# Kernel optimization log

Measured on AMD Instinct MI355X. Metric: run time of the kernel, lower is better.

The kernel has to match this reference:

```python
import jax, jax.numpy as jnp
import numpy as np

N_HEAD = 16
ROPE_BASE = 10000.0


def _rope_cache(T, head_dim):
    # half-split RoPE: cos/sin of shape [T, head_dim//2]
    half = head_dim // 2
    inv_freq = ROPE_BASE ** (-jnp.arange(half, dtype=jnp.float32) / half)
    angles = jnp.arange(T, dtype=jnp.float32)[:, None] * inv_freq[None, :]  # [T, half]
    return jnp.cos(angles), jnp.sin(angles)


def _apply_rope(x, cos, sin):
    # x: [B, H, T, D]; cos/sin: [T, D//2]
    half = x.shape[-1] // 2
    x1, x2 = x[..., :half], x[..., half:]
    c = cos[None, None, :, :]
    s = sin[None, None, :, :]
    return jnp.concatenate([x1 * c - x2 * s, x1 * s + x2 * c], axis=-1)


def setup_inputs() -> dict:
    key = jax.random.key(0)
    k1, k2, k3 = jax.random.split(key, 3)
    B, T, C = 2, 2048, 1024
    x = jax.random.normal(k1, (B, T, C), dtype=jnp.float32)
    w_attn = jax.random.normal(k2, (C, 3 * C), dtype=jnp.float32) * (C ** -0.5)
    b_attn = jnp.zeros((3 * C,), dtype=jnp.float32)
    w_proj = jax.random.normal(k3, (C, C), dtype=jnp.float32) * (C ** -0.5)
    b_proj = jnp.zeros((C,), dtype=jnp.float32)
    return {"x": x, "w_attn": w_attn, "b_attn": b_attn, "w_proj": w_proj, "b_proj": b_proj}


def reference(x, w_attn, b_attn, w_proj, b_proj):
    B, T, C = x.shape
    H = N_HEAD
    hd = C // H

    qkv = x @ w_attn + b_attn                      # [B, T, 3C] fused QKV
    q, k, v = jnp.split(qkv, 3, axis=-1)
    q = q.reshape(B, T, H, hd).transpose(0, 2, 1, 3)  # [B, H, T, hd]
    k = k.reshape(B, T, H, hd).transpose(0, 2, 1, 3)
    v = v.reshape(B, T, H, hd).transpose(0, 2, 1, 3)

    cos, sin = _rope_cache(T, hd)
    q = _apply_rope(q, cos, sin)
    k = _apply_rope(k, cos, sin)

    scale = 1.0 / jnp.sqrt(jnp.float32(hd))
    att = jnp.einsum("bhqd,bhkd->bhqk", q, k) * scale  # [B, H, T, T]
    causal = jnp.tril(jnp.ones((T, T), dtype=bool))
    att = jnp.where(causal[None, None], att, -jnp.inf)
    att = jax.nn.softmax(att, axis=-1)
    y = jnp.einsum("bhqk,bhkd->bhqd", att, v)          # [B, H, T, hd]
    y = y.transpose(0, 2, 1, 3).reshape(B, T, C)
    return y @ w_proj + b_proj
```

## Files before the change

kernel.cpp:

```cpp
#include <hip/hip_runtime.h>
#include <hip/hip_bf16.h>
#include <cmath>

typedef _Float16 half_t;
typedef half_t half4 __attribute__((ext_vector_type(4)));
typedef half_t half8 __attribute__((ext_vector_type(8)));
typedef float f32x4 __attribute__((ext_vector_type(4)));

#define N_HEADS 16
#define HD      64
#define T_SEQ   2048
#define B_SZ    2
#define C_DIM   1024
#define M_ROWS  (B_SZ * T_SEQ)
#define N_QKV   (3 * C_DIM)
#define QSCALE  0.18033688f

__device__ inline void load_lds16(const half_t* g, half_t* l) {
  __builtin_amdgcn_global_load_lds(
      (const __attribute__((address_space(1))) void*)g,
      (__attribute__((address_space(3))) void*)l, 16, 0, 0);
}

__global__ __launch_bounds__(256) void k_prep(const float* __restrict__ x,
                                              half_t* __restrict__ xb,
                                              const float* __restrict__ wa,
                                              half_t* __restrict__ wT,
                                              const float* __restrict__ wp,
                                              half_t* __restrict__ wpT,
                                              float2* __restrict__ tbl) {
  __shared__ float tile[64][65];
  int bid = blockIdx.x, tid = threadIdx.x;
  if (bid < 4096) {
    int i = (bid * 256 + tid) * 4;
    float4 v = *(const float4*)(x + i);
    half_t o[4] = {(half_t)v.x, (half_t)v.y, (half_t)v.z, (half_t)v.w};
    *(ulong1*)(xb + i) = *(ulong1*)o;
    return;
  }
  if (bid >= 5120) {
    int idx = (bid - 5120) * 256 + tid;
    int t = idx >> 5, j = idx & 31;
    float inv = exp2f(-(float)j * (13.287712379549449f / 32.0f));
    float s, c;
    sincosf((float)t * inv, &s, &c);
    tbl[idx] = make_float2(c, s);
    return;
  }
  const float* in; half_t* out; int K, N, id;
  if (bid < 4864) { id = bid - 4096; in = wa; out = wT;  K = 1024; N = 3072; }
  else            { id = bid - 4864; in = wp; out = wpT; K = 1024; N = 1024; }
  int n0 = (id % (N / 64)) * 64, k0 = (id / (N / 64)) * 64;
  int tx = tid & 63, ty = tid >> 6;
  #pragma unroll
  for (int i = 0; i < 64; i += 4)
    tile[ty + i][tx] = in[(size_t)(k0 + ty + i) * N + n0 + tx];
  __syncthreads();
  #pragma unroll
  for (int i = 0; i < 64; i += 4) {
    int r = ty + i;
    out[(size_t)(n0 + r) * K + k0 + tx] = (half_t)tile[tx][r];
  }
}

template <typename OT, int TN>
__global__ __launch_bounds__(256) void k_gemm(const half_t* __restrict__ A,
                                              const half_t* __restrict__ Bt,
                                              const float* __restrict__ bias,
                                              OT* __restrict__ C,
                                              int M, int N, int K) {
  constexpr int NI = TN / 32;
  __shared__ half_t As[128 * 64];
  __shared__ half_t Bs[TN * 64];
  int tid = threadIdx.x;
  int wave = tid >> 6, lane = tid & 63;
  int lane15 = lane & 15, quad = lane >> 4;
  int wm = (wave >> 1) * 64, wn = (wave & 1) * (TN / 2);
  int bm0 = blockIdx.y * 128, bn0 = blockIdx.x * TN;
  f32x4 acc[4][NI] = {};

  for (int kb = 0; kb < K; kb += 64) {
    const half_t* Ag = A + (size_t)bm0 * K + kb;
    const half_t* Bg = Bt + (size_t)bn0 * K + kb;
    __syncthreads();
    #pragma unroll
    for (int p = 0; p < 4; p++) {
      int fc = wave * 4 * 64 + p * 64 + lane;
      int r = fc >> 3, c = (fc & 7) ^ (r & 7);
      load_lds16(Ag + (size_t)r * K + c * 8, As + (wave * 4 + p) * 512);
    }
    #pragma unroll
    for (int p = 0; p < NI; p++) {
      int fc = wave * NI * 64 + p * 64 + lane;
      int r = fc >> 3, c = (fc & 7) ^ (r & 7);
      load_lds16(Bg + (size_t)r * K + c * 8, Bs + (wave * NI + p) * 512);
    }
    __syncthreads();
    #pragma unroll
    for (int ks = 0; ks < 2; ks++) {
      half8 af[4], bf[NI];
      #pragma unroll
      for (int i = 0; i < 4; i++) {
        int Ra = wm + i * 16 + lane15;
        af[i] = *(const half8*)(As + Ra * 64 + ((ks * 4 + quad) ^ (Ra & 7)) * 8);
      }
      #pragma unroll
      for (int i = 0; i < NI; i++) {
        int Rb = wn + i * 16 + lane15;
        bf[i] = *(const half8*)(Bs + Rb * 64 + ((ks * 4 + quad) ^ (Rb & 7)) * 8);
      }
      #pragma unroll
      for (int mi = 0; mi < 4; mi++)
        #pragma unroll
        for (int ni = 0; ni < NI; ni++)
          acc[mi][ni] = __builtin_amdgcn_mfma_f32_16x16x32_f16(af[mi], bf[ni], acc[mi][ni], 0, 0, 0);
    }
  }
  #pragma unroll
  for (int mi = 0; mi < 4; mi++)
    #pragma unroll
    for (int ni = 0; ni < NI; ni++) {
      int n = bn0 + wn + ni * 16 + lane15;
      float bv = bias[n];
      int mrow = bm0 + wm + mi * 16 + quad * 4;
      #pragma unroll
      for (int r = 0; r < 4; r++)
        C[(size_t)(mrow + r) * N + n] = (OT)(acc[mi][ni][r] + bv);
    }
}

__global__ __launch_bounds__(256) void k_gemm_qkv(const half_t* __restrict__ A,
                                                  const half_t* __restrict__ Bt,
                                                  const float* __restrict__ bias,
                                                  const float2* __restrict__ tbl,
                                                  half_t* __restrict__ Qo,
                                                  half_t* __restrict__ Ko,
                                                  half_t* __restrict__ Vo) {
  __shared__ half_t smem[16640];
  half_t* As = smem;
  half_t* Bs = smem + 8192;
  int tid = threadIdx.x;
  int wave = tid >> 6, lane = tid & 63;
  int lane15 = lane & 15, quad = lane >> 4;
  int wm = (wave >> 1) * 64, wn = (wave & 1) * 64;
  int bm0 = blockIdx.y * 128, bn0 = blockIdx.x * 128;
  f32x4 acc[4][4] = {};

  for (int kb = 0; kb < C_DIM; kb += 64) {
    const half_t* Ag = A + (size_t)bm0 * C_DIM + kb;
    const half_t* Bg = Bt + (size_t)bn0 * C_DIM + kb;
    __syncthreads();
    #pragma unroll
    for (int p = 0; p < 4; p++) {
      int fc = wave * 4 * 64 + p * 64 + lane;
      int r = fc >> 3, c = (fc & 7) ^ (r & 7);
      load_lds16(Ag + (size_t)r * C_DIM + c * 8, As + (wave * 4 + p) * 512);
    }
    #pragma unroll
    for (int p = 0; p < 4; p++) {
      int fc = wave * 4 * 64 + p * 64 + lane;
      int r = fc >> 3, c = (fc & 7) ^ (r & 7);
      load_lds16(Bg + (size_t)r * C_DIM + c * 8, Bs + (wave * 4 + p) * 512);
    }
    __syncthreads();
    #pragma unroll
    for (int ks = 0; ks < 2; ks++) {
      half8 af[4], bf[4];
      #pragma unroll
      for (int i = 0; i < 4; i++) {
        int Ra = wm + i * 16 + lane15;
        af[i] = *(const half8*)(As + Ra * 64 + ((ks * 4 + quad) ^ (Ra & 7)) * 8);
      }
      #pragma unroll
      for (int i = 0; i < 4; i++) {
        int Rb = wn + i * 16 + lane15;
        bf[i] = *(const half8*)(Bs + Rb * 64 + ((ks * 4 + quad) ^ (Rb & 7)) * 8);
      }
      #pragma unroll
      for (int mi = 0; mi < 4; mi++)
        #pragma unroll
        for (int ni = 0; ni < 4; ni++)
          acc[mi][ni] = __builtin_amdgcn_mfma_f32_16x16x32_f16(af[mi], bf[ni], acc[mi][ni], 0, 0, 0);
    }
  }
  #pragma unroll
  for (int ni = 0; ni < 4; ni++) {
    float bv = bias[bn0 + wn + ni * 16 + lane15];
    #pragma unroll
    for (int mi = 0; mi < 4; mi++)
      #pragma unroll
      for (int r = 0; r < 4; r++) acc[mi][ni][r] += bv;
  }

  int third = bn0 >> 10;
  if (third < 2) {
    half_t* Ob = (third == 0) ? Qo : Ko;
    int h = ((bn0 & 1023) + wn) >> 6;
    #pragma unroll
    for (int mi = 0; mi < 4; mi++) {
      int mrow = bm0 + wm + mi * 16 + quad * 4;
      int bq = mrow >> 11, tq = mrow & 2047;
      half_t* outp = Ob + ((size_t)(bq * 16 + h) * T_SEQ + tq) * HD;
      #pragma unroll
      for (int p = 0; p < 2; p++) {
        int j = p * 16 + lane15;
        #pragma unroll
        for (int r = 0; r < 4; r++) {
          float2 cs = tbl[(tq + r) * 32 + j];
          float a1 = acc[mi][p][r], a2 = acc[mi][p + 2][r];
          float o1 = a1 * cs.x - a2 * cs.y;
          float o2 = a1 * cs.y + a2 * cs.x;
          if (third == 0) { o1 *= QSCALE; o2 *= QSCALE; }
          outp[r * HD + j]      = (half_t)o1;
          outp[r * HD + j + 32] = (half_t)o2;
        }
      }
    }
  } else {
    __syncthreads();
    #pragma unroll
    for (int mi = 0; mi < 4; mi++)
      #pragma unroll
      for (int ni = 0; ni < 4; ni++) {
        int tl = wm + mi * 16 + quad * 4, nl = wn + ni * 16 + lane15;
        #pragma unroll
        for (int r = 0; r < 4; r++)
          smem[(tl + r) * 130 + nl] = (half_t)acc[mi][ni][r];
      }
    __syncthreads();
    int hV = (bn0 - 2048) >> 6;
    int bq = bm0 >> 11, tq0 = bm0 & 2047;
    int c8 = (tid & 7) * 8;
    #pragma unroll
    for (int p = 0; p < 8; p++) {
      int gr = p * 32 + (tid >> 3);
      int tb = gr & 1, d = (gr >> 1) & 63, h2 = gr >> 7;
      half8 vv;
      #pragma unroll
      for (int jj = 0; jj < 8; jj++)
        vv[jj] = smem[(tb * 64 + c8 + jj) * 130 + h2 * 64 + d];
      *(half8*)(Vo + ((size_t)((bq * 16 + hV + h2) * 32 + (tq0 >> 6) + tb) * 64 + d) * 64 + c8) = vv;
    }
  }
}

template <bool DIAG>
__device__ __forceinline__ void tile_mfma(const half_t* __restrict__ Kt,
                                          const half_t* __restrict__ Vt,
                                          half8 bq0, half8 bq1,
                                          f32x4 (&ot)[4], float& l,
                                          int lane15, int quad, int qloc) {
  f32x4 sacc[4];
  #pragma unroll
  for (int s = 0; s < 4; s++) {
    int R_ = s * 16 + lane15;
    half8 ak0 = *(const half8*)(Kt + R_ * 64 + ((quad) ^ (R_ & 7)) * 8);
    half8 ak1 = *(const half8*)(Kt + R_ * 64 + ((4 + quad) ^ (R_ & 7)) * 8);
    f32x4 z = {};
    z = __builtin_amdgcn_mfma_f32_16x16x32_f16(ak0, bq0, z, 0, 0, 0);
    sacc[s] = __builtin_amdgcn_mfma_f32_16x16x32_f16(ak1, bq1, z, 0, 0, 0);
  }
  #pragma unroll
  for (int s = 0; s < 4; s++) {
    half4 bp;
    #pragma unroll
    for (int r = 0; r < 4; r++) {
      float sv = sacc[s][r];
      if (DIAG && (s * 16 + quad * 4 + r > qloc)) sv = -1.0e30f;
      float p = exp2f(fminf(sv, 14.0f));
      l += p;
      bp[r] = (half_t)p;
    }
    #pragma unroll
    for (int nm = 0; nm < 4; nm++) {
      int Rv = nm * 16 + lane15;
      half4 av = *(const half4*)(Vt + Rv * 64 +
                                 ((2 * s + (quad >> 1)) ^ (Rv & 7)) * 8 +
                                 (quad & 1) * 4);
      ot[nm] = __builtin_amdgcn_mfma_f32_16x16x16f16(av, bp, ot[nm], 0, 0, 0);
    }
  }
}

#define STAGE(bb, t_)                                                          \
  {                                                                            \
    int gS = wave >> 3;                                                        \
    int idx = (wave & 7) * 64 + lane;                                          \
    int rr_ = idx >> 3, cc = (idx & 7) ^ (rr_ & 7);                            \
    int j = 2 * (t_) + gS;                                                     \
    load_lds16(Kb + (size_t)(j * 64 + rr_) * HD + cc * 8,                      \
               &KV[bb][0][gS][0] + idx * 8);                                   \
    load_lds16(Vb + (size_t)j * 4096 + rr_ * 64 + cc * 8,                      \
               &KV[bb][1][gS][0] + idx * 8);                                   \
  }

__device__ __forceinline__ void process_tile(
    int qt, const half_t* __restrict__ Qb, const half_t* __restrict__ Kb,
    const half_t* __restrict__ Vb, half_t* __restrict__ y, int b, int h,
    half_t (&KV)[2][2][2][4096],
    int wave, int lane, int g, int wq, int lane15, int quad) {
  int q0 = qt * 128;
  int qrow = q0 + wq * 16 + lane15;
  half8 bq0 = *(const half8*)(Qb + (size_t)qrow * HD + quad * 8);
  half8 bq1 = *(const half8*)(Qb + (size_t)qrow * HD + 32 + quad * 8);
  f32x4 ot[4] = {};
  float l = 0.f;
  int R = qt + 1;
  for (int r = 0; r < R - 1; r++) {
    __syncthreads();
    STAGE((r + 1) & 1, r + 1);
    tile_mfma<false>(&KV[r & 1][0][g][0], &KV[r & 1][1][g][0], bq0, bq1, ot, l,
                     lane15, quad, 0);
  }
  __syncthreads();
  {
    int buf = (R - 1) & 1;
    const half_t* Kt = &KV[buf][0][g][0];
    const half_t* Vt = &KV[buf][1][g][0];
    if (g == 0)
      tile_mfma<true>(Kt, Vt, bq0, bq1, ot, l, lane15, quad, wq * 16 + lane15);
    else if (wq >= 4)
      tile_mfma<true>(Kt, Vt, bq0, bq1, ot, l, lane15, quad,
                      (wq - 4) * 16 + lane15);
  }
  l += __shfl_xor(l, 16);
  l += __shfl_xor(l, 32);
  __syncthreads();
  float* cb = (float*)&KV[0][0][0][0];
  int ci = (wq * 64 + lane) * 17;
  if (g == 1) {
    #pragma unroll
    for (int nm = 0; nm < 4; nm++)
      #pragma unroll
      for (int r = 0; r < 4; r++) cb[ci + nm * 4 + r] = ot[nm][r];
    cb[ci + 16] = l;
  }
  __syncthreads();
  if (g == 0) {
    #pragma unroll
    for (int nm = 0; nm < 4; nm++)
      #pragma unroll
      for (int r = 0; r < 4; r++) ot[nm][r] += cb[ci + nm * 4 + r];
    l += cb[ci + 16];
    float invl = 1.0f / l;
    int t = q0 + wq * 16 + lane15;
    half_t* yr = y + (size_t)(b * T_SEQ + t) * C_DIM + h * 64;
    #pragma unroll
    for (int nm = 0; nm < 4; nm++) {
      half4 o4;
      #pragma unroll
      for (int r = 0; r < 4; r++) o4[r] = (half_t)(ot[nm][r] * invl);
      *(half4*)(yr + nm * 16 + quad * 4) = o4;
    }
  }
  __syncthreads();
}

__global__ __launch_bounds__(1024, 4) void k_flash(const half_t* __restrict__ Qg,
                                                   const half_t* __restrict__ Kg,
                                                   const half_t* __restrict__ Vg,
                                                   half_t* __restrict__ y) {
  __shared__ half_t KV[2][2][2][4096];
  int bh = blockIdx.y;
  int b = bh >> 4, h = bh & 15;
  int x = blockIdx.x;
  int tid = threadIdx.x;
  int wave = tid >> 6, lane = tid & 63;
  int g = wave >> 3, wq = wave & 7;
  int lane15 = lane & 15, quad = lane >> 4;
  const half_t* Qb = Qg + (size_t)bh * T_SEQ * HD;
  const half_t* Kb = Kg + (size_t)bh * T_SEQ * HD;
  const half_t* Vb = Vg + (size_t)bh * HD * T_SEQ;

  int qtA = x, qtB = 15 - x;
  STAGE(0, 0);
  process_tile(qtA, Qb, Kb, Vb, y, b, h, KV, wave, lane, g, wq, lane15, quad);
  STAGE(0, 0);
  process_tile(qtB, Qb, Kb, Vb, y, b, h, KV, wave, lane, g, wq, lane15, quad);
  #undef STAGE
}

extern "C" void kernel_launch(void* const* d_in, const int* in_sizes, int n_in,
                              void* d_out, int out_size, void* d_ws, size_t ws_size,
                              hipStream_t stream) {
  const float* x      = (const float*)d_in[0];
  const float* w_attn = (const float*)d_in[1];
  const float* b_attn = (const float*)d_in[2];
  const float* w_proj = (const float*)d_in[3];
  const float* b_proj = (const float*)d_in[4];
  float* out = (float*)d_out;

  char* ws = (char*)d_ws;
  const size_t MB = 1u << 20;
  half_t* xb  = (half_t*)(ws);
  half_t* wT  = (half_t*)(ws + 8 * MB);
  half_t* wpT = (half_t*)(ws + 14 * MB);
  half_t* Q   = (half_t*)(ws + 16 * MB);
  half_t* Kb  = (half_t*)(ws + 24 * MB);
  half_t* Vt  = (half_t*)(ws + 32 * MB);
  half_t* y   = (half_t*)(ws + 40 * MB);
  float2* tbl = (float2*)(ws + 48 * MB);

  k_prep<<<4096 + 768 + 256 + 256, 256, 0, stream>>>(x, xb, w_attn, wT,
                                                     w_proj, wpT, tbl);
  k_gemm_qkv<<<dim3(N_QKV / 128, M_ROWS / 128), 256, 0, stream>>>(
      xb, wT, b_attn, tbl, Q, Kb, Vt);
  k_flash<<<dim3(8, B_SZ * N_HEADS), 1024, 0, stream>>>(Q, Kb, Vt, y);
  k_gemm<float, 64><<<dim3(C_DIM / 64, M_ROWS / 128), 256, 0, stream>>>(
      y, wpT, b_proj, out, M_ROWS, C_DIM, C_DIM);
}
```

Before: 185.6 us.

## Double-buffer LDS tiles in QKV and projection GEMMs to overlap loads with MFMA

Both GEMM kernels now keep two LDS buffers for the A and B tiles. The async global-to-LDS loads for the next k-tile are issued before the MFMA work on the current tile, and one barrier per iteration replaces two. The aim is to hide global load latency behind matrix math. In exchange, LDS use per block roughly doubles (64KB in the QKV kernel), which can lower occupancy. The V-transpose epilogue reuses the first buffer as scratch.

```diff
diff --git a/kernel.cpp b/kernel.cpp
--- a/kernel.cpp
+++ b/kernel.cpp
@@ -70,8 +70,8 @@
                                               OT* __restrict__ C,
                                               int M, int N, int K) {
   constexpr int NI = TN / 32;
-  __shared__ half_t As[128 * 64];
-  __shared__ half_t Bs[TN * 64];
+  __shared__ half_t As[2][128 * 64];
+  __shared__ half_t Bs[2][TN * 64];
   int tid = threadIdx.x;
   int wave = tid >> 6, lane = tid & 63;
   int lane15 = lane & 15, quad = lane >> 4;
@@ -79,35 +79,43 @@
   int bm0 = blockIdx.y * 128, bn0 = blockIdx.x * TN;
   f32x4 acc[4][NI] = {};
 
-  for (int kb = 0; kb < K; kb += 64) {
-    const half_t* Ag = A + (size_t)bm0 * K + kb;
-    const half_t* Bg = Bt + (size_t)bn0 * K + kb;
+#define G_STAGE(bb, kb)                                                        \
+  {                                                                            \
+    const half_t* Ag = A + (size_t)bm0 * K + (kb);                             \
+    const half_t* Bg = Bt + (size_t)bn0 * K + (kb);                            \
+    _Pragma("unroll")                                                          \
+    for (int p = 0; p < 4; p++) {                                              \
+      int fc = wave * 4 * 64 + p * 64 + lane;                                  \
+      int r = fc >> 3, c = (fc & 7) ^ (r & 7);                                 \
+      load_lds16(Ag + (size_t)r * K + c * 8, &As[bb][0] + (wave * 4 + p) * 512); \
+    }                                                                          \
+    _Pragma("unroll")                                                          \
+    for (int p = 0; p < NI; p++) {                                             \
+      int fc = wave * NI * 64 + p * 64 + lane;                                 \
+      int r = fc >> 3, c = (fc & 7) ^ (r & 7);                                 \
+      load_lds16(Bg + (size_t)r * K + c * 8, &Bs[bb][0] + (wave * NI + p) * 512); \
+    }                                                                          \
+  }
+
+  G_STAGE(0, 0);
+  int NT = K / 64;
+  for (int kt = 0; kt < NT; kt++) {
     __syncthreads();
-    #pragma unroll
-    for (int p = 0; p < 4; p++) {
-      int fc = wave * 4 * 64 + p * 64 + lane;
-      int r = fc >> 3, c = (fc & 7) ^ (r & 7);
-      load_lds16(Ag + (size_t)r * K + c * 8, As + (wave * 4 + p) * 512);
-    }
-    #pragma unroll
-    for (int p = 0; p < NI; p++) {
-      int fc = wave * NI * 64 + p * 64 + lane;
-      int r = fc >> 3, c = (fc & 7) ^ (r & 7);
-      load_lds16(Bg + (size_t)r * K + c * 8, Bs + (wave * NI + p) * 512);
-    }
-    __syncthreads();
+    if (kt + 1 < NT) G_STAGE((kt + 1) & 1, (kt + 1) * 64);
+    const half_t* Asb = &As[kt & 1][0];
+    const half_t* Bsb = &Bs[kt & 1][0];
     #pragma unroll
     for (int ks = 0; ks < 2; ks++) {
       half8 af[4], bf[NI];
       #pragma unroll
       for (int i = 0; i < 4; i++) {
         int Ra = wm + i * 16 + lane15;
-        af[i] = *(const half8*)(As + Ra * 64 + ((ks * 4 + quad) ^ (Ra & 7)) * 8);
+        af[i] = *(const half8*)(Asb + Ra * 64 + ((ks * 4 + quad) ^ (Ra & 7)) * 8);
       }
       #pragma unroll
       for (int i = 0; i < NI; i++) {
         int Rb = wn + i * 16 + lane15;
-        bf[i] = *(const half8*)(Bs + Rb * 64 + ((ks * 4 + quad) ^ (Rb & 7)) * 8);
+        bf[i] = *(const half8*)(Bsb + Rb * 64 + ((ks * 4 + quad) ^ (Rb & 7)) * 8);
       }
       #pragma unroll
       for (int mi = 0; mi < 4; mi++)
@@ -116,6 +124,7 @@
           acc[mi][ni] = __builtin_amdgcn_mfma_f32_16x16x32_f16(af[mi], bf[ni], acc[mi][ni], 0, 0, 0);
     }
   }
+#undef G_STAGE
   #pragma unroll
   for (int mi = 0; mi < 4; mi++)
     #pragma unroll
@@ -136,9 +145,7 @@
                                                   half_t* __restrict__ Qo,
                                                   half_t* __restrict__ Ko,
                                                   half_t* __restrict__ Vo) {
-  __shared__ half_t smem[16640];
-  half_t* As = smem;
-  half_t* Bs = smem + 8192;
+  __shared__ half_t smem[2][16384];
   int tid = threadIdx.x;
   int wave = tid >> 6, lane = tid & 63;
   int lane15 = lane & 15, quad = lane >> 4;
@@ -146,23 +153,27 @@
   int bm0 = blockIdx.y * 128, bn0 = blockIdx.x * 128;
   f32x4 acc[4][4] = {};
 
-  for (int kb = 0; kb < C_DIM; kb += 64) {
-    const half_t* Ag = A + (size_t)bm0 * C_DIM + kb;
-    const half_t* Bg = Bt + (size_t)bn0 * C_DIM + kb;
+#define QKV_STAGE(bb, kb)                                                      \
+  {                                                                            \
+    const half_t* Ag = A + (size_t)bm0 * C_DIM + (kb);                         \
+    const half_t* Bg = Bt + (size_t)bn0 * C_DIM + (kb);                        \
+    _Pragma("unroll")                                                          \
+    for (int p = 0; p < 4; p++) {                                              \
+      int fc = wave * 4 * 64 + p * 64 + lane;                                  \
+      int r = fc >> 3, c = (fc & 7) ^ (r & 7);                                 \
+      load_lds16(Ag + (size_t)r * C_DIM + c * 8,                               \
+                 &smem[bb][0] + (wave * 4 + p) * 512);                         \
+      load_lds16(Bg + (size_t)r * C_DIM + c * 8,                               \
+                 &smem[bb][8192] + (wave * 4 + p) * 512);                      \
+    }                                                                          \
+  }
+
+  QKV_STAGE(0, 0);
+  for (int kt = 0; kt < 16; kt++) {
     __syncthreads();
-    #pragma unroll
-    for (int p = 0; p < 4; p++) {
-      int fc = wave * 4 * 64 + p * 64 + lane;
-      int r = fc >> 3, c = (fc & 7) ^ (r & 7);
-      load_lds16(Ag + (size_t)r * C_DIM + c * 8, As + (wave * 4 + p) * 512);
-    }
-    #pragma unroll
-    for (int p = 0; p < 4; p++) {
-      int fc = wave * 4 * 64 + p * 64 + lane;
-      int r = fc >> 3, c = (fc & 7) ^ (r & 7);
-      load_lds16(Bg + (size_t)r * C_DIM + c * 8, Bs + (wave * 4 + p) * 512);
-    }
-    __syncthreads();
+    if (kt < 15) QKV_STAGE((kt + 1) & 1, (kt + 1) * 64);
+    const half_t* As = &smem[kt & 1][0];
+    const half_t* Bs = &smem[kt & 1][8192];
     #pragma unroll
     for (int ks = 0; ks < 2; ks++) {
       half8 af[4], bf[4];
@@ -183,6 +194,7 @@
           acc[mi][ni] = __builtin_amdgcn_mfma_f32_16x16x32_f16(af[mi], bf[ni], acc[mi][ni], 0, 0, 0);
     }
   }
+#undef QKV_STAGE
   #pragma unroll
   for (int ni = 0; ni < 4; ni++) {
     float bv = bias[bn0 + wn + ni * 16 + lane15];
@@ -218,6 +230,7 @@
     }
   } else {
     __syncthreads();
+    half_t* vt = &smem[0][0];
     #pragma unroll
     for (int mi = 0; mi < 4; mi++)
       #pragma unroll
@@ -225,7 +238,7 @@
         int tl = wm + mi * 16 + quad * 4, nl = wn + ni * 16 + lane15;
         #pragma unroll
         for (int r = 0; r < 4; r++)
-          smem[(tl + r) * 130 + nl] = (half_t)acc[mi][ni][r];
+          vt[(tl + r) * 130 + nl] = (half_t)acc[mi][ni][r];
       }
     __syncthreads();
     int hV = (bn0 - 2048) >> 6;
@@ -238,7 +251,7 @@
       half8 vv;
       #pragma unroll
       for (int jj = 0; jj < 8; jj++)
-        vv[jj] = smem[(tb * 64 + c8 + jj) * 130 + h2 * 64 + d];
+        vv[jj] = vt[(tb * 64 + c8 + jj) * 130 + h2 * 64 + d];
       *(half8*)(Vo + ((size_t)((bq * 16 + hV + h2) * 32 + (tq0 >> 6) + tb) * 64 + d) * 64 + c8) = vv;
     }
   }
```

Result: no change. 184.2 us (-0.8%).
